# Performance work log

Measured on AMD Instinct MI355X. Metric: run time of the kernel, lower is better.

## Reference

```python
import jax, jax.numpy as jnp
import numpy as np

N = 4_194_304
H = 20
P = 10.0
MOMENTUM = 0.1


def setup_inputs() -> dict:
    key = jax.random.key(0)
    ks = jax.random.split(key, 12)
    w = 0.01  # init window from initialize_optimizer_params
    inp = {
        "grad_t": jax.random.normal(ks[0], (N, 1), dtype=jnp.float32),
        "loss_t": jnp.full((N, 1), 1.2345, dtype=jnp.float32),  # scalar loss broadcast
        "f_tm1": jnp.ones((N, 1), dtype=jnp.float32),
        "i_tm1": jnp.zeros((N, 1), dtype=jnp.float32),
        "theta_tm1": jax.random.normal(ks[1], (N, 1), dtype=jnp.float32) * np.sqrt(2.0 / N).astype(np.float32),
        "delta_tm1": jnp.zeros((N, 1), dtype=jnp.float32),
        "h0": jnp.zeros((N, H), dtype=jnp.float32),
        "c0": jnp.zeros((N, H), dtype=jnp.float32),
        "W_ih": jax.random.uniform(ks[2], (4 * H, 4), jnp.float32, -w, w),
        "W_hh": jax.random.uniform(ks[3], (4 * H, H), jnp.float32, -w, w),
        "b_ih": jax.random.uniform(ks[4], (4 * H,), jnp.float32, -w, w),
        "b_hh": jax.random.uniform(ks[5], (4 * H,), jnp.float32, -w, w),
        "W_theta_w": jax.random.uniform(ks[6], (1, H + 2), jnp.float32, -w, w),
        "W_theta_b": jax.random.uniform(ks[7], (1,), jnp.float32, 4.0, 5.0),
        "W_grad_w": jax.random.uniform(ks[8], (1, H + 2), jnp.float32, -w, w),
        "W_grad_b": jax.random.uniform(ks[9], (1,), jnp.float32, -5.0, -4.0),
    }
    return inp


def _preprocess(x):
    # x: [N]; returns [N, 2] with (log|x|/p or -1, sign(x) or x*e^p)
    eps = np.exp(-P).astype(np.float32)
    big = np.exp(P).astype(np.float32)
    ax = jnp.abs(x)
    cond = ax >= eps
    safe = jnp.where(cond, ax, 1.0)
    z1 = jnp.where(cond, jnp.log(safe) / P, -1.0)
    z2 = jnp.where(cond, jnp.sign(x), x * big)
    return jnp.stack([z1, z2], axis=-1)


def reference(grad_t, loss_t, f_tm1, i_tm1, theta_tm1, delta_tm1, h0, c0,
              W_ih, W_hh, b_ih, b_hh, W_theta_w, W_theta_b, W_grad_w, W_grad_b):
    # LSTM input: concat(preprocess(grad), preprocess(loss)) -> [N, 4]
    x = jnp.concatenate([_preprocess(grad_t[:, 0]), _preprocess(loss_t[:, 0])], axis=-1)
    # single LSTM step (PyTorch gate order i, f, g, o)
    gates = x @ W_ih.T + h0 @ W_hh.T + (b_ih + b_hh)  # [N, 4H]
    ig, fg, gg, og = jnp.split(gates, 4, axis=-1)
    ig = jax.nn.sigmoid(ig)
    fg = jax.nn.sigmoid(fg)
    gg = jnp.tanh(gg)
    og = jax.nn.sigmoid(og)
    c_t = fg * c0 + ig * gg
    h_t = og * jnp.tanh(c_t)  # [N, H] == output_t
    # gating heads: Linear(H+2 -> 1) + sigmoid
    f_in = jnp.concatenate([h_t, theta_tm1, f_tm1], axis=-1)  # [N, H+2]
    i_in = jnp.concatenate([h_t, theta_tm1, i_tm1], axis=-1)
    f_t = jax.nn.sigmoid(f_in @ W_theta_w.T + W_theta_b)  # [N, 1]
    i_t = jax.nn.sigmoid(i_in @ W_grad_w.T + W_grad_b)
    # gated momentum update
    delta_t = MOMENTUM * delta_tm1 - i_t * grad_t
    theta_t = f_t * theta_tm1 + delta_t
    return theta_t
```

## Files before the change

### kernel.cpp

```cpp
#include <hip/hip_runtime.h>

#define NP 16
#define WAVES 4
#define BLK (WAVES*64)

typedef __bf16 bf16x8 __attribute__((ext_vector_type(8)));
typedef float  f32x4  __attribute__((ext_vector_type(4)));

__device__ __forceinline__ float ex2(float x){ return __builtin_amdgcn_exp2f(x); }
__device__ __forceinline__ float rcp_(float x){ return __builtin_amdgcn_rcpf(x); }
__device__ __forceinline__ float lg2(float x){ return __builtin_amdgcn_logf(x); }

#define LOG2E      1.4426950408889634f
#define TWOLOG2E   2.8853900817779268f
#define LN2_OVER_P 0.06931471805599453f
#define NEG_PL2E  -14.426950408889634f
#define EPSP       4.5399929762484854e-05f
#define EXPP       22026.465794806718f

struct Raw {
    float  g, lv;
    float4 hA, hB;
    float  c[5];
    float  th, ff, ii, dl;
};

__global__ __launch_bounds__(BLK) void lstm_opt_mfma(
    const float* __restrict__ grad, const float* __restrict__ loss,
    const float* __restrict__ f1,   const float* __restrict__ i1,
    const float* __restrict__ th1,  const float* __restrict__ dl1,
    const float* __restrict__ h0,   const float* __restrict__ c0,
    const float* __restrict__ Wih,  const float* __restrict__ Whh,
    const float* __restrict__ bih,  const float* __restrict__ bhh,
    const float* __restrict__ Wtw,  const float* __restrict__ Wtb,
    const float* __restrict__ Wgw,  const float* __restrict__ Wgb,
    float* __restrict__ out)
{
    const int tid  = threadIdx.x;
    const int lane = tid & 63;
    const int wid  = tid >> 6;
    const int e16  = lane & 15;
    const int grp  = lane >> 4;

    bf16x8 af[5];
    f32x4  bias4[5];
    float  wtwv[5], wgwv[5];
    {
        const int gate = e16 & 3;
        const int jA0  = 5 * (e16 >> 2);
        const float sg = (gate == 2) ? TWOLOG2E : -LOG2E;
        #pragma unroll
        for (int t = 0; t < 5; ++t) {
            const int r = gate*20 + (jA0 + t);
            float wf[8];
            #pragma unroll
            for (int i = 0; i < 8; ++i) {
                const int k = grp*8 + i;
                float v = 0.0f;
                if (k < 20)      v = Whh[r*20 + k];
                else if (k < 24) {
                    v = Wih[r*4 + (k - 20)];
                    if (k == 20 || k == 22) v *= LN2_OVER_P;
                }
                wf[i] = v * sg;
            }
            union { unsigned u[4]; bf16x8 v; } pk;
            #pragma unroll
            for (int q = 0; q < 4; ++q) {
                unsigned r_;
                asm("v_cvt_pk_bf16_f32 %0, %1, %2" : "=v"(r_) : "v"(wf[2*q]), "v"(wf[2*q+1]));
                pk.u[q] = r_;
            }
            af[t] = pk.v;

            const int jj = 5*grp + t;
            f32x4 b;
            #pragma unroll
            for (int m = 0; m < 4; ++m) {
                const float sm = (m == 2) ? TWOLOG2E : -LOG2E;
                b[m] = (bih[m*20 + jj] + bhh[m*20 + jj]) * sm;
            }
            bias4[t] = b;
            wtwv[t] = Wtw[jj];
            wgwv[t] = Wgw[jj];
        }
    }
    const float wt20 = Wtw[20], wt21 = Wtw[21], tb = Wtb[0];
    const float wg20 = Wgw[20], wg21 = Wgw[21], gb = Wgb[0];

    const int o0   = (grp == 0) ? 0 : (grp == 1) ? 8  : 16;
    const int o1   = (grp == 0) ? 4 : (grp == 1) ? 12 : 16;
    const int cOff = 5 * grp;
    const int waveBase = (blockIdx.x * WAVES + wid) * (16 * NP);

    auto loadR = [&](Raw& S, int p) {
        const int e = waveBase + p*16 + e16;
        S.g  = grad[e];
        S.lv = loss[e];
        const float* hp = h0 + (size_t)e * 20;
        S.hA = *(const float4*)(hp + o0);
        S.hB = *(const float4*)(hp + o1);
        const float* cp = c0 + (size_t)e * 20 + cOff;
        #pragma unroll
        for (int i = 0; i < 5; ++i) S.c[i] = cp[i];
        S.th = th1[e];
        S.ff = f1[e];
        S.ii = i1[e];
        S.dl = dl1[e];
    };

    auto computeR = [&](const Raw& S, int p) {
        const int e = waveBase + p*16 + e16;

        const float g = S.g, lv = S.lv;
        const float ax = fabsf(g);
        const bool  cg = ax >= EPSP;
        const float u0 = cg ? lg2(ax) : NEG_PL2E;
        const float x1 = cg ? copysignf(1.0f, g) : g * EXPP;
        const float al = fabsf(lv);
        const bool  cl = al >= EPSP;
        const float u2 = cl ? lg2(al) : NEG_PL2E;
        const float x3 = cl ? copysignf(1.0f, lv) : lv * EXPP;

        const bool z = (grp == 3);
        const float fa0 = z ? 0.0f : S.hA.x, fa1 = z ? 0.0f : S.hA.y;
        const float fa2 = z ? 0.0f : S.hA.z, fa3 = z ? 0.0f : S.hA.w;
        float fb0, fb1, fb2, fb3;
        if (grp == 2)      { fb0 = u0;  fb1 = x1;  fb2 = u2;  fb3 = x3; }
        else if (z)        { fb0 = 0.f; fb1 = 0.f; fb2 = 0.f; fb3 = 0.f; }
        else               { fb0 = S.hB.x; fb1 = S.hB.y; fb2 = S.hB.z; fb3 = S.hB.w; }

        union { unsigned u[4]; bf16x8 v; } bp;
        {
            unsigned r0, r1, r2, r3;
            asm("v_cvt_pk_bf16_f32 %0, %1, %2" : "=v"(r0) : "v"(fa0), "v"(fa1));
            asm("v_cvt_pk_bf16_f32 %0, %1, %2" : "=v"(r1) : "v"(fa2), "v"(fa3));
            asm("v_cvt_pk_bf16_f32 %0, %1, %2" : "=v"(r2) : "v"(fb0), "v"(fb1));
            asm("v_cvt_pk_bf16_f32 %0, %1, %2" : "=v"(r3) : "v"(fb2), "v"(fb3));
            bp.u[0] = r0; bp.u[1] = r1; bp.u[2] = r2; bp.u[3] = r3;
        }
        const bf16x8 bfrag = bp.v;

        f32x4 acc[5];
        #pragma unroll
        for (int t = 0; t < 5; ++t)
            acc[t] = __builtin_amdgcn_mfma_f32_16x16x32_bf16(af[t], bfrag, bias4[t], 0, 0, 0);

        float fac = 0.0f, iac = 0.0f;
        #pragma unroll
        for (int t = 0; t < 5; ++t) {
            const float si = rcp_(1.0f + ex2(acc[t][0]));
            const float sf = rcp_(1.0f + ex2(acc[t][1]));
            const float tg = 1.0f - 2.0f * rcp_(1.0f + ex2(acc[t][2]));
            const float so = rcp_(1.0f + ex2(acc[t][3]));
            const float ct = sf * S.c[t] + si * tg;
            const float ht = so * (1.0f - 2.0f * rcp_(1.0f + ex2(TWOLOG2E * ct)));
            fac += ht * wtwv[t];
            iac += ht * wgwv[t];
        }
        fac += __shfl_xor(fac, 16); fac += __shfl_xor(fac, 32);
        iac += __shfl_xor(iac, 16); iac += __shfl_xor(iac, 32);

        if (grp == 0) {
            const float ft = rcp_(1.0f + ex2(-LOG2E * (fac + tb + S.th*wt20 + S.ff*wt21)));
            const float it = rcp_(1.0f + ex2(-LOG2E * (iac + gb + S.th*wg20 + S.ii*wg21)));
            out[e] = ft*S.th + 0.1f*S.dl - it*g;
        }
    };

    Raw R0, R1;
    loadR(R0, 0);
    loadR(R1, 1);
    __builtin_amdgcn_sched_barrier(0);

    #pragma unroll 1
    for (int p = 0; p < NP; p += 2) {
        computeR(R0, p);
        const int pa = (p + 2 < NP) ? (p + 2) : (NP - 1);
        loadR(R0, pa);
        __builtin_amdgcn_sched_barrier(0);

        computeR(R1, p + 1);
        const int pb = (p + 3 < NP) ? (p + 3) : (NP - 1);
        loadR(R1, pb);
        __builtin_amdgcn_sched_barrier(0);
    }
}

extern "C" void kernel_launch(void* const* d_in, const int* in_sizes, int n_in,
                              void* d_out, int out_size, void* d_ws, size_t ws_size,
                              hipStream_t stream) {
    const float* grad = (const float*)d_in[0];
    const float* loss = (const float*)d_in[1];
    const float* f1   = (const float*)d_in[2];
    const float* i1   = (const float*)d_in[3];
    const float* th1  = (const float*)d_in[4];
    const float* dl1  = (const float*)d_in[5];
    const float* h0   = (const float*)d_in[6];
    const float* c0   = (const float*)d_in[7];
    const float* Wih  = (const float*)d_in[8];
    const float* Whh  = (const float*)d_in[9];
    const float* bih  = (const float*)d_in[10];
    const float* bhh  = (const float*)d_in[11];
    const float* Wtw  = (const float*)d_in[12];
    const float* Wtb  = (const float*)d_in[13];
    const float* Wgw  = (const float*)d_in[14];
    const float* Wgb  = (const float*)d_in[15];

    const int N = in_sizes[0];
    const int blocks = N / (16 * NP * WAVES);
    hipLaunchKernelGGL(lstm_opt_mfma, dim3(blocks), dim3(BLK), 0, stream,
                       grad, loss, f1, i1, th1, dl1, h0, c0,
                       Wih, Whh, bih, bhh, Wtw, Wtb, Wgw, Wgb,
                       (float*)d_out);
}
```

Baseline: 206.0 us.

## Stage h0/c0 rows through LDS with async global_load_lds double buffering

Each wave now copies the contiguous 16-row slab of h0 and c0 into its own LDS region using coalesced `global_load_lds` DMA (16-byte per-lane chunks plus a 4-byte tail). Lanes then read their strided h and c fragments from LDS instead of making scattered global loads. The goal is fully coalesced global traffic for the dominant h0/c0 stream, with the next tile prefetched into a second buffer while the current tile is computed. In exchange, register prefetch depth drops from two tiles to one, and correctness depends on the compiler inserting the vmcnt waits needed for the LDS DMA.

```diff
diff --git a/kernel.cpp b/kernel.cpp
--- a/kernel.cpp
+++ b/kernel.cpp
@@ -18,12 +18,11 @@
 #define EPSP       4.5399929762484854e-05f
 #define EXPP       22026.465794806718f
 
-struct Raw {
-    float  g, lv;
-    float4 hA, hB;
-    float  c[5];
-    float  th, ff, ii, dl;
-};
+#define AS1C(p) (const __attribute__((address_space(1))) void*)(p)
+#define AS3(p)  (__attribute__((address_space(3))) void*)(p)
+
+struct Scal { float g, lv, th, ff, ii, dl; };
+
 
 __global__ __launch_bounds__(BLK) void lstm_opt_mfma(
     const float* __restrict__ grad, const float* __restrict__ loss,
@@ -36,11 +35,15 @@
     const float* __restrict__ Wgw,  const float* __restrict__ Wgb,
     float* __restrict__ out)
 {
+    __shared__ __align__(16) float lds[WAVES * 1280];
+
     const int tid  = threadIdx.x;
     const int lane = tid & 63;
     const int wid  = tid >> 6;
     const int e16  = lane & 15;
     const int grp  = lane >> 4;
+
+    float* const wls = lds + wid * 1280;
 
     bf16x8 af[5];
     f32x4  bias4[5];
@@ -88,29 +91,46 @@
     const float wt20 = Wtw[20], wt21 = Wtw[21], tb = Wtb[0];
     const float wg20 = Wgw[20], wg21 = Wgw[21], gb = Wgb[0];
 
-    const int o0   = (grp == 0) ? 0 : (grp == 1) ? 8  : 16;
-    const int o1   = (grp == 0) ? 4 : (grp == 1) ? 12 : 16;
-    const int cOff = 5 * grp;
+    const int o0 = (grp == 0) ? 0 : (grp == 1) ? 8  : 16;
+    const int o1 = (grp == 0) ? 4 : (grp == 1) ? 12 : 16;
     const int waveBase = (blockIdx.x * WAVES + wid) * (16 * NP);
 
-    auto loadR = [&](Raw& S, int p) {
+    auto stage = [&](int p, int b) {
+        const size_t rowBase = (size_t)(waveBase + p*16) * 20;
+        const float* hs = h0 + rowBase;
+        const float* cs = c0 + rowBase;
+        float* hd = wls + b*640;
+        float* cd = hd + 320;
+        __builtin_amdgcn_global_load_lds(AS1C(hs + 4*lane),       AS3(hd),       16, 0, 0);
+        __builtin_amdgcn_global_load_lds(AS1C(hs + 256 + lane),   AS3(hd + 256),  4, 0, 0);
+        __builtin_amdgcn_global_load_lds(AS1C(cs + 4*lane),       AS3(cd),       16, 0, 0);
+        __builtin_amdgcn_global_load_lds(AS1C(cs + 256 + lane),   AS3(cd + 256),  4, 0, 0);
+    };
+
+    auto loadS = [&](Scal& S, int p) {
         const int e = waveBase + p*16 + e16;
         S.g  = grad[e];
         S.lv = loss[e];
-        const float* hp = h0 + (size_t)e * 20;
-        S.hA = *(const float4*)(hp + o0);
-        S.hB = *(const float4*)(hp + o1);
-        const float* cp = c0 + (size_t)e * 20 + cOff;
-        #pragma unroll
-        for (int i = 0; i < 5; ++i) S.c[i] = cp[i];
         S.th = th1[e];
         S.ff = f1[e];
         S.ii = i1[e];
         S.dl = dl1[e];
     };
 
-    auto computeR = [&](const Raw& S, int p) {
-        const int e = waveBase + p*16 + e16;
+    auto body = [&](int p, int b, const Scal& S, Scal& Snext) {
+        float* hb = wls + b*640;
+        const float* hp = hb + 20*e16;
+        const float4 hA = *(const float4*)(hp + o0);
+        const float4 hB = *(const float4*)(hp + o1);
+        const float* cp = hb + 320 + 20*e16 + 5*grp;
+        float c5[5];
+        #pragma unroll
+        for (int t = 0; t < 5; ++t) c5[t] = cp[t];
+
+        if (p + 1 < NP) {
+            stage(p + 1, b ^ 1);
+            loadS(Snext, p + 1);
+        }
 
         const float g = S.g, lv = S.lv;
         const float ax = fabsf(g);
@@ -123,12 +143,12 @@
         const float x3 = cl ? copysignf(1.0f, lv) : lv * EXPP;
 
         const bool z = (grp == 3);
-        const float fa0 = z ? 0.0f : S.hA.x, fa1 = z ? 0.0f : S.hA.y;
-        const float fa2 = z ? 0.0f : S.hA.z, fa3 = z ? 0.0f : S.hA.w;
+        const float fa0 = z ? 0.0f : hA.x, fa1 = z ? 0.0f : hA.y;
+        const float fa2 = z ? 0.0f : hA.z, fa3 = z ? 0.0f : hA.w;
         float fb0, fb1, fb2, fb3;
         if (grp == 2)      { fb0 = u0;  fb1 = x1;  fb2 = u2;  fb3 = x3; }
         else if (z)        { fb0 = 0.f; fb1 = 0.f; fb2 = 0.f; fb3 = 0.f; }
-        else               { fb0 = S.hB.x; fb1 = S.hB.y; fb2 = S.hB.z; fb3 = S.hB.w; }
+        else               { fb0 = hB.x; fb1 = hB.y; fb2 = hB.z; fb3 = hB.w; }
 
         union { unsigned u[4]; bf16x8 v; } bp;
         {
@@ -153,7 +173,7 @@
             const float sf = rcp_(1.0f + ex2(acc[t][1]));
             const float tg = 1.0f - 2.0f * rcp_(1.0f + ex2(acc[t][2]));
             const float so = rcp_(1.0f + ex2(acc[t][3]));
-            const float ct = sf * S.c[t] + si * tg;
+            const float ct = sf * c5[t] + si * tg;
             const float ht = so * (1.0f - 2.0f * rcp_(1.0f + ex2(TWOLOG2E * ct)));
             fac += ht * wtwv[t];
             iac += ht * wgwv[t];
@@ -162,28 +182,20 @@
         iac += __shfl_xor(iac, 16); iac += __shfl_xor(iac, 32);
 
         if (grp == 0) {
+            const int e = waveBase + p*16 + e16;
             const float ft = rcp_(1.0f + ex2(-LOG2E * (fac + tb + S.th*wt20 + S.ff*wt21)));
             const float it = rcp_(1.0f + ex2(-LOG2E * (iac + gb + S.th*wg20 + S.ii*wg21)));
             out[e] = ft*S.th + 0.1f*S.dl - it*g;
         }
     };
 
-    Raw R0, R1;
-    loadR(R0, 0);
-    loadR(R1, 1);
-    __builtin_amdgcn_sched_barrier(0);
-
+    Scal S0, S1;
+    stage(0, 0);
+    loadS(S0, 0);
     #pragma unroll 1
     for (int p = 0; p < NP; p += 2) {
-        computeR(R0, p);
-        const int pa = (p + 2 < NP) ? (p + 2) : (NP - 1);
-        loadR(R0, pa);
-        __builtin_amdgcn_sched_barrier(0);
-
-        computeR(R1, p + 1);
-        const int pb = (p + 3 < NP) ? (p + 3) : (NP - 1);
-        loadR(R1, pb);
-        __builtin_amdgcn_sched_barrier(0);
+        body(p,     0, S0, S1);
+        body(p + 1, 1, S1, S0);
     }
 }
 
```

Result: no change. 206.6 us (+0.3%).

## Fold LSTM bias into MFMA K dimension and shorten register prefetch pipeline

Applied to the files above, without the earlier changes.

Moves the combined LSTM gate bias into an unused K slot (k=24) of the bf16 weight fragment and feeds a constant 1.0 in the matching B element, so the MFMA accumulators start from zero and the five bias4 f32x4 registers go away. It also changes the prefetch from two buffers fully in flight to a staggered load/compute order, removes the sched_barriers, and requests 6 waves per EU through launch_bounds. The aim is to cut VGPR pressure and raise occupancy to hide memory latency. In exchange the bias is now rounded to bf16, and the compiler is free to reorder loads around compute.

```diff
diff --git a/kernel.cpp b/kernel.cpp
--- a/kernel.cpp
+++ b/kernel.cpp
@@ -25,7 +25,7 @@
     float  th, ff, ii, dl;
 };
 
-__global__ __launch_bounds__(BLK) void lstm_opt_mfma(
+__global__ __launch_bounds__(BLK, 6) void lstm_opt_mfma(
     const float* __restrict__ grad, const float* __restrict__ loss,
     const float* __restrict__ f1,   const float* __restrict__ i1,
     const float* __restrict__ th1,  const float* __restrict__ dl1,
@@ -43,7 +43,6 @@
     const int grp  = lane >> 4;
 
     bf16x8 af[5];
-    f32x4  bias4[5];
     float  wtwv[5], wgwv[5];
     {
         const int gate = e16 & 3;
@@ -51,7 +50,8 @@
         const float sg = (gate == 2) ? TWOLOG2E : -LOG2E;
         #pragma unroll
         for (int t = 0; t < 5; ++t) {
-            const int r = gate*20 + (jA0 + t);
+            const int jrow = jA0 + t;
+            const int r = gate*20 + jrow;
             float wf[8];
             #pragma unroll
             for (int i = 0; i < 8; ++i) {
@@ -62,6 +62,7 @@
                     v = Wih[r*4 + (k - 20)];
                     if (k == 20 || k == 22) v *= LN2_OVER_P;
                 }
+                else if (k == 24) v = bih[r] + bhh[r];
                 wf[i] = v * sg;
             }
             union { unsigned u[4]; bf16x8 v; } pk;
@@ -74,13 +75,6 @@
             af[t] = pk.v;
 
             const int jj = 5*grp + t;
-            f32x4 b;
-            #pragma unroll
-            for (int m = 0; m < 4; ++m) {
-                const float sm = (m == 2) ? TWOLOG2E : -LOG2E;
-                b[m] = (bih[m*20 + jj] + bhh[m*20 + jj]) * sm;
-            }
-            bias4[t] = b;
             wtwv[t] = Wtw[jj];
             wgwv[t] = Wgw[jj];
         }
@@ -123,8 +117,10 @@
         const float x3 = cl ? copysignf(1.0f, lv) : lv * EXPP;
 
         const bool z = (grp == 3);
-        const float fa0 = z ? 0.0f : S.hA.x, fa1 = z ? 0.0f : S.hA.y;
-        const float fa2 = z ? 0.0f : S.hA.z, fa3 = z ? 0.0f : S.hA.w;
+        const float fa0 = z ? 1.0f : S.hA.x;
+        const float fa1 = z ? 0.0f : S.hA.y;
+        const float fa2 = z ? 0.0f : S.hA.z;
+        const float fa3 = z ? 0.0f : S.hA.w;
         float fb0, fb1, fb2, fb3;
         if (grp == 2)      { fb0 = u0;  fb1 = x1;  fb2 = u2;  fb3 = x3; }
         else if (z)        { fb0 = 0.f; fb1 = 0.f; fb2 = 0.f; fb3 = 0.f; }
@@ -143,8 +139,10 @@
 
         f32x4 acc[5];
         #pragma unroll
-        for (int t = 0; t < 5; ++t)
-            acc[t] = __builtin_amdgcn_mfma_f32_16x16x32_bf16(af[t], bfrag, bias4[t], 0, 0, 0);
+        for (int t = 0; t < 5; ++t) {
+            const f32x4 zero = {0.0f, 0.0f, 0.0f, 0.0f};
+            acc[t] = __builtin_amdgcn_mfma_f32_16x16x32_bf16(af[t], bfrag, zero, 0, 0, 0);
+        }
 
         float fac = 0.0f, iac = 0.0f;
         #pragma unroll
@@ -170,20 +168,13 @@
 
     Raw R0, R1;
     loadR(R0, 0);
-    loadR(R1, 1);
-    __builtin_amdgcn_sched_barrier(0);
-
     #pragma unroll 1
     for (int p = 0; p < NP; p += 2) {
+        loadR(R1, p + 1);
         computeR(R0, p);
-        const int pa = (p + 2 < NP) ? (p + 2) : (NP - 1);
-        loadR(R0, pa);
-        __builtin_amdgcn_sched_barrier(0);
-
+        const int pn = (p + 2 < NP) ? (p + 2) : (NP - 1);
+        loadR(R0, pn);
         computeR(R1, p + 1);
-        const int pb = (p + 3 < NP) ? (p + 3) : (NP - 1);
-        loadR(R1, pb);
-        __builtin_amdgcn_sched_barrier(0);
     }
 }
 
```

Result: slower. 281.8 us (+36.8%).
